# Kernel tuning notes

Hardware: AMD Instinct MI355X
Metric: run time of the kernel (lower is better)

Reference implementation:

```python
import jax, jax.numpy as jnp
import numpy as np

N = 100000   # nodes
E = 1600000  # edges
D_IN = 128
H = 64
L = 3        # num SAGE layers
G = 512      # graphs in batch


def setup_inputs() -> dict:
    key = jax.random.key(0)
    ks = jax.random.split(key, 12)
    s = 0.05
    return {
        "x": jax.random.normal(ks[0], (N, D_IN), dtype=jnp.float32),
        "edge_index": jax.random.randint(ks[1], (2, E), 0, N, dtype=jnp.int64),
        "edge_attr": jax.random.normal(ks[2], (E, 1), dtype=jnp.float32),
        "batch": jnp.sort(jax.random.randint(ks[3], (N,), 0, G, dtype=jnp.int64)),
        "W0": jax.random.normal(ks[4], (D_IN, H), dtype=jnp.float32) * s,
        "b0": jnp.zeros((H,), dtype=jnp.float32),
        "Wl": jax.random.normal(ks[5], (L, H, H), dtype=jnp.float32) * s,  # lin_l (aggregated neighbors), has bias
        "bl": jnp.zeros((L, H), dtype=jnp.float32),
        "Wr": jax.random.normal(ks[6], (L, H, H), dtype=jnp.float32) * s,  # lin_r (root), no bias
        "W1": jax.random.normal(ks[7], (H, H), dtype=jnp.float32) * s,
        "b1": jnp.zeros((H,), dtype=jnp.float32),
    }


def reference(x, edge_index, edge_attr, batch, W0, b0, Wl, bl, Wr, W1, b1):
    # edge_attr is accepted but unused, matching the torch module.
    h = jax.nn.relu(x @ W0 + b0)                    # [N, H]
    src, dst = edge_index[0], edge_index[1]
    ones_e = jnp.ones((E,), dtype=h.dtype)
    deg = jax.ops.segment_sum(ones_e, dst, num_segments=N)
    deg = jnp.clip(deg, 1.0)[:, None]               # avoid div by zero (PyG mean -> 0 for isolated)
    for i in range(L):
        # SAGEConv: mean-aggregate source features onto targets, then lin_l(agg)+lin_r(h)
        agg = jax.ops.segment_sum(h[src], dst, num_segments=N) / deg  # [N, H]
        h = jax.nn.relu(agg @ Wl[i] + bl[i] + h @ Wr[i])
    # global_mean_pool over batch ids
    cnt = jax.ops.segment_sum(jnp.ones((N,), dtype=h.dtype), batch, num_segments=G)
    pooled = jax.ops.segment_sum(h, batch, num_segments=G) / jnp.clip(cnt, 1.0)[:, None]  # [G, H]
    return pooled @ W1 + b1                          # [G, H]
```

## Files before the change

### kernel.cpp

```cpp
#include <hip/hip_runtime.h>
#include <hip/hip_bf16.h>

#define NN 100000
#define NE 1600000
#define DIN 128
#define NG 512
#define MAXD 64
#define NBUK 391
#define BCAP 5120
#define CHUNK ((NE + NBUK - 1) / NBUK)
#define NTILE ((NN + 63) >> 6)

typedef __attribute__((ext_vector_type(8))) __bf16 bf16x8;
typedef __attribute__((ext_vector_type(4))) float f32x4;

static __device__ __forceinline__ unsigned short bfhi(float f) {
    __hip_bfloat16 h = __float2bfloat16(f);
    return *reinterpret_cast<unsigned short*>(&h);
}
static __device__ __forceinline__ float bf2f(unsigned short u) {
    unsigned v = (unsigned)u << 16;
    return __uint_as_float(v);
}
static __device__ __forceinline__ bf16x8 ldfrag(const void* p) {
    bf16x8 r;
    __builtin_memcpy(&r, p, 16);
    return r;
}
static __device__ __forceinline__ int swz(int a) {
    return a ^ (((a >> 8) & 3) << 5) ^ (((a >> 12) & 3) << 4);
}


#define GB 256
__global__ void __launch_bounds__(512) k_front(const int* __restrict__ src,
                                               const int* __restrict__ dst,
                                               int* __restrict__ cursor,
                                               unsigned int* __restrict__ bucket,
                                               const float* __restrict__ x,
                                               const float* __restrict__ W0,
                                               const float* __restrict__ b0,
                                               float* __restrict__ h) {
    __shared__ unsigned short sS[2 * 8192];
    __shared__ int lcnt[NBUK];
    __shared__ int lbase[NBUK];
    if (blockIdx.x < NBUK) {
        for (int i = threadIdx.x; i < NBUK; i += 512) lcnt[i] = 0;
        __syncthreads();
        int e0 = blockIdx.x * CHUNK;
        int e1 = min(e0 + CHUNK, NE);
        for (int e = e0 + (int)threadIdx.x; e < e1; e += 512)
            atomicAdd(&lcnt[dst[e] >> 8], 1);
        __syncthreads();
        for (int i = threadIdx.x; i < NBUK; i += 512) {
            int c = lcnt[i];
            lbase[i] = c ? atomicAdd(&cursor[i], c) : 0;
            lcnt[i] = 0;
        }
        __syncthreads();
        for (int e = e0 + (int)threadIdx.x; e < e1; e += 512) {
            int d = dst[e];
            int s = src[e];
            int bk = d >> 8;
            int pos = lbase[bk] + atomicAdd(&lcnt[bk], 1);
            if (pos < BCAP)
                bucket[(size_t)bk * BCAP + pos] = ((unsigned)s << 8) | (unsigned)(d & 255);
        }
    } else {
        unsigned short* sP0 = sS;
        unsigned short* sP1 = sS + 8192;
        for (int i = threadIdx.x; i < 8192; i += 512) {
            int k = i >> 6, c = i & 63;
            int slot = ((k >> 5) << 2) | (c >> 4);
            int ln   = (((k >> 3) & 3) << 4) | (c & 15);
            int ba   = swz((((((slot << 6) | ln) << 3) | (k & 7)) << 1));
            float w0 = W0[i];
            unsigned short hh = bfhi(w0);
            *(unsigned short*)((char*)sP0 + ba) = hh;
            *(unsigned short*)((char*)sP1 + ba) = bfhi(w0 - bf2f(hh));
        }
        __syncthreads();
        int lane = threadIdx.x & 63;
        int wv   = threadIdx.x >> 6;
        int cb   = wv & 3;
        int rbh  = wv >> 2;
        int col  = (cb << 4) | (lane & 15);
        float bj = b0[col];
        int r0   = (lane >> 4) << 2;
        bf16x8 Bh[4], Bl[4];
#pragma unroll
        for (int ks = 0; ks < 4; ++ks) {
            int bb = swz(((((ks << 2) | cb) << 6) | lane) << 4);
            Bh[ks] = ldfrag((const char*)sP0 + bb);
            Bl[ks] = ldfrag((const char*)sP1 + bb);
        }
        for (int t = blockIdx.x - NBUK; t < NTILE; t += GB) {
            int n0 = t << 6;
            __syncthreads();
#pragma unroll
            for (int i = 0; i < 4; ++i) {
                int tau = (int)threadIdx.x + (i << 9);
                int r = tau >> 5, kq = tau & 31;
                int n = n0 + r;
                float4 v = make_float4(0.f, 0.f, 0.f, 0.f);
                if (n < NN) v = *(const float4*)(x + ((size_t)n << 7) + (kq << 2));
                int k0   = kq << 2;
                int slot = ((k0 >> 5) << 2) | (r >> 4);
                int ln   = (((k0 >> 3) & 3) << 4) | (r & 15);
                int ba   = swz((((((slot << 6) | ln) << 3) | (k0 & 7)) << 1));
                unsigned short h0 = bfhi(v.x), h1 = bfhi(v.y),
                               h2 = bfhi(v.z), h3 = bfhi(v.w);
                *(ushort4*)((char*)sP0 + ba) = make_ushort4(h0, h1, h2, h3);
                *(ushort4*)((char*)sP1 + ba) = make_ushort4(
                    bfhi(v.x - bf2f(h0)), bfhi(v.y - bf2f(h1)),
                    bfhi(v.z - bf2f(h2)), bfhi(v.w - bf2f(h3)));
            }
            __syncthreads();
            f32x4 acc[2] = {{0.f,0.f,0.f,0.f},{0.f,0.f,0.f,0.f}};
#pragma unroll
            for (int ks = 0; ks < 4; ++ks) {
#pragma unroll
                for (int rl = 0; rl < 2; ++rl) {
                    int rb = (rbh << 1) | rl;
                    int ab = swz(((((ks << 2) | rb) << 6) | lane) << 4);
                    bf16x8 ah = ldfrag((const char*)sP0 + ab);
                    bf16x8 al = ldfrag((const char*)sP1 + ab);
                    acc[rl] = __builtin_amdgcn_mfma_f32_16x16x32_bf16(ah, Bh[ks], acc[rl], 0, 0, 0);
                    acc[rl] = __builtin_amdgcn_mfma_f32_16x16x32_bf16(ah, Bl[ks], acc[rl], 0, 0, 0);
                    acc[rl] = __builtin_amdgcn_mfma_f32_16x16x32_bf16(al, Bh[ks], acc[rl], 0, 0, 0);
                }
            }
#pragma unroll
            for (int rl = 0; rl < 2; ++rl) {
                int rb = (rbh << 1) | rl;
#pragma unroll
                for (int reg = 0; reg < 4; ++reg) {
                    int row = (rb << 4) + r0 + reg;
                    int n = n0 + row;
                    if (n < NN)
                        h[((size_t)n << 6) + col] = fmaxf(acc[rl][reg] + bj, 0.f);
                }
            }
        }
    }
}

__device__ __forceinline__ void gemmLR_mfma(unsigned short* sS,
                                            int tid, int nblk, int bidx,
                                            float* __restrict__ h_r,
                                            __hip_bfloat16* __restrict__ g,
                                            const float* __restrict__ Wl,
                                            const float* __restrict__ bl,
                                            const float* __restrict__ Wr) {
    unsigned short* sP0 = sS;
    unsigned short* sP1 = sS + 4096;
    int lane = tid & 63;
    int cb   = tid >> 6;
    bf16x8 BLh[2], BLl[2], BRh[2], BRl[2];
    for (int i = tid; i < 4096; i += 256) {
        int k = i >> 6, c = i & 63;
        int slot = ((k >> 5) << 2) | (c >> 4);
        int ln   = (((k >> 3) & 3) << 4) | (c & 15);
        int ba   = swz((((((slot << 6) | ln) << 3) | (k & 7)) << 1));
        float w = Wl[i];
        unsigned short hh = bfhi(w);
        *(unsigned short*)((char*)sP0 + ba) = hh;
        *(unsigned short*)((char*)sP1 + ba) = bfhi(w - bf2f(hh));
    }
    __syncthreads();
#pragma unroll
    for (int ks = 0; ks < 2; ++ks) {
        int bb = swz(((((ks << 2) | cb) << 6) | lane) << 4);
        BLh[ks] = ldfrag((const char*)sP0 + bb);
        BLl[ks] = ldfrag((const char*)sP1 + bb);
    }
    __syncthreads();
    for (int i = tid; i < 4096; i += 256) {
        int k = i >> 6, c = i & 63;
        int slot = ((k >> 5) << 2) | (c >> 4);
        int ln   = (((k >> 3) & 3) << 4) | (c & 15);
        int ba   = swz((((((slot << 6) | ln) << 3) | (k & 7)) << 1));
        float w = Wr[i];
        unsigned short hh = bfhi(w);
        *(unsigned short*)((char*)sP0 + ba) = hh;
        *(unsigned short*)((char*)sP1 + ba) = bfhi(w - bf2f(hh));
    }
    __syncthreads();
#pragma unroll
    for (int ks = 0; ks < 2; ++ks) {
        int bb = swz(((((ks << 2) | cb) << 6) | lane) << 4);
        BRh[ks] = ldfrag((const char*)sP0 + bb);
        BRl[ks] = ldfrag((const char*)sP1 + bb);
    }
    int col = (cb << 4) | (lane & 15);
    float bj = bl[col];
    int r0  = (lane >> 4) << 2;
    unsigned short* gp = (unsigned short*)g;
    for (int t = bidx; t < NTILE; t += nblk) {
        int n0 = t << 6;
        __syncthreads();
#pragma unroll
        for (int i = 0; i < 4; ++i) {
            int tau = tid + (i << 8);
            int r = tau >> 4, kq = tau & 15;
            int n = n0 + r;
            float4 v = make_float4(0.f, 0.f, 0.f, 0.f);
            if (n < NN) v = *(const float4*)(h_r + ((size_t)n << 6) + (kq << 2));
            int k0   = kq << 2;
            int slot = ((k0 >> 5) << 2) | (r >> 4);
            int ln   = (((k0 >> 3) & 3) << 4) | (r & 15);
            int ba   = swz((((((slot << 6) | ln) << 3) | (k0 & 7)) << 1));
            unsigned short h0 = bfhi(v.x), h1 = bfhi(v.y),
                           h2 = bfhi(v.z), h3 = bfhi(v.w);
            *(ushort4*)((char*)sP0 + ba) = make_ushort4(h0, h1, h2, h3);
            *(ushort4*)((char*)sP1 + ba) = make_ushort4(
                bfhi(v.x - bf2f(h0)), bfhi(v.y - bf2f(h1)),
                bfhi(v.z - bf2f(h2)), bfhi(v.w - bf2f(h3)));
        }
        __syncthreads();
        f32x4 accl[4] = {{0.f,0.f,0.f,0.f},{0.f,0.f,0.f,0.f},
                         {0.f,0.f,0.f,0.f},{0.f,0.f,0.f,0.f}};
        f32x4 accr[4] = {{0.f,0.f,0.f,0.f},{0.f,0.f,0.f,0.f},
                         {0.f,0.f,0.f,0.f},{0.f,0.f,0.f,0.f}};
#pragma unroll
        for (int ks = 0; ks < 2; ++ks) {
#pragma unroll
            for (int rb = 0; rb < 4; ++rb) {
                int ab = swz(((((ks << 2) | rb) << 6) | lane) << 4);
                bf16x8 ah = ldfrag((const char*)sP0 + ab);
                bf16x8 al = ldfrag((const char*)sP1 + ab);
                accl[rb] = __builtin_amdgcn_mfma_f32_16x16x32_bf16(ah, BLh[ks], accl[rb], 0, 0, 0);
                accl[rb] = __builtin_amdgcn_mfma_f32_16x16x32_bf16(ah, BLl[ks], accl[rb], 0, 0, 0);
                accl[rb] = __builtin_amdgcn_mfma_f32_16x16x32_bf16(al, BLh[ks], accl[rb], 0, 0, 0);
                accr[rb] = __builtin_amdgcn_mfma_f32_16x16x32_bf16(ah, BRh[ks], accr[rb], 0, 0, 0);
                accr[rb] = __builtin_amdgcn_mfma_f32_16x16x32_bf16(ah, BRl[ks], accr[rb], 0, 0, 0);
                accr[rb] = __builtin_amdgcn_mfma_f32_16x16x32_bf16(al, BRh[ks], accr[rb], 0, 0, 0);
            }
        }
#pragma unroll
        for (int rb = 0; rb < 4; ++rb) {
#pragma unroll
            for (int reg = 0; reg < 4; ++reg) {
                int row = (rb << 4) + r0 + reg;
                int n = n0 + row;
                if (n < NN) {
                    size_t o = ((size_t)n << 6) + col;
                    gp[o]  = bfhi(accl[rb][reg]);
                    h_r[o] = accr[rb][reg] + bj;
                }
            }
        }
    }
}

#define MGB 512
__global__ void __launch_bounds__(256) k_mid(const unsigned int* __restrict__ bucket,
                                             const int* __restrict__ cursor,
                                             int* __restrict__ cnt,
                                             int* __restrict__ ell,
                                             float* __restrict__ h_r,
                                             __hip_bfloat16* __restrict__ g,
                                             const float* __restrict__ Wl,
                                             const float* __restrict__ bl,
                                             const float* __restrict__ Wr) {
    __shared__ unsigned short sS[2 * 4096];
    __shared__ int lc[256];
    if (blockIdx.x < NBUK) {
        lc[threadIdx.x] = 0;
        int b = blockIdx.x;
        __syncthreads();
        int m = min(cursor[b], BCAP);
        const unsigned int* bp = bucket + (size_t)b * BCAP;
        for (int i = threadIdx.x; i < m; i += 256) {
            unsigned v = bp[i];
            int dlo = (int)(v & 255u);
            int s   = (int)(v >> 8);
            int p   = atomicAdd(&lc[dlo], 1);
            if (p < MAXD)
                ell[(((size_t)b << 8) + dlo) * MAXD + p] = s;
        }
        __syncthreads();
        int n = (b << 8) + (int)threadIdx.x;
        if (n < NN) cnt[n] = lc[threadIdx.x];
    } else {
        gemmLR_mfma(sS, threadIdx.x, MGB, blockIdx.x - NBUK, h_r, g, Wl, bl, Wr);
    }
}

#define ACCU(U) { \
    a0 += __uint_as_float((U).x << 16); a1 += __uint_as_float((U).x & 0xffff0000u); \
    a2 += __uint_as_float((U).y << 16); a3 += __uint_as_float((U).y & 0xffff0000u); \
    a4 += __uint_as_float((U).z << 16); a5 += __uint_as_float((U).z & 0xffff0000u); \
    a6 += __uint_as_float((U).w << 16); a7 += __uint_as_float((U).w & 0xffff0000u); }

#define FB 512
__global__ void __launch_bounds__(512) k_gg(const uint4* __restrict__ gin,
                                            float* __restrict__ rA,
                                            unsigned short* __restrict__ gout,
                                            const int* __restrict__ cnt,
                                            const int* __restrict__ ell,
                                            const float* __restrict__ Wl,
                                            const float* __restrict__ bl,
                                            const float* __restrict__ Wr) {
    __shared__ unsigned short sS[2 * 4096];
    unsigned short* sP0 = sS;
    unsigned short* sP1 = sS + 4096;
    int tid = (int)threadIdx.x;
    int lane = tid & 63;
    int w    = tid >> 6;
    int cb   = w & 3;
    int rbh  = w >> 2;
    bf16x8 BLh[2], BLl[2], BRh[2], BRl[2];
    for (int i = tid; i < 4096; i += 512) {
        int k = i >> 6, c = i & 63;
        int slot = ((k >> 5) << 2) | (c >> 4);
        int ln   = (((k >> 3) & 3) << 4) | (c & 15);
        int ba   = swz((((((slot << 6) | ln) << 3) | (k & 7)) << 1));
        float wv_ = Wl[i];
        unsigned short hh = bfhi(wv_);
        *(unsigned short*)((char*)sP0 + ba) = hh;
        *(unsigned short*)((char*)sP1 + ba) = bfhi(wv_ - bf2f(hh));
    }
    __syncthreads();
#pragma unroll
    for (int ks = 0; ks < 2; ++ks) {
        int bb = swz(((((ks << 2) | cb) << 6) | lane) << 4);
        BLh[ks] = ldfrag((const char*)sP0 + bb);
        BLl[ks] = ldfrag((const char*)sP1 + bb);
    }
    __syncthreads();
    for (int i = tid; i < 4096; i += 512) {
        int k = i >> 6, c = i & 63;
        int slot = ((k >> 5) << 2) | (c >> 4);
        int ln   = (((k >> 3) & 3) << 4) | (c & 15);
        int ba   = swz((((((slot << 6) | ln) << 3) | (k & 7)) << 1));
        float wv_ = Wr[i];
        unsigned short hh = bfhi(wv_);
        *(unsigned short*)((char*)sP0 + ba) = hh;
        *(unsigned short*)((char*)sP1 + ba) = bfhi(wv_ - bf2f(hh));
    }
    __syncthreads();
#pragma unroll
    for (int ks = 0; ks < 2; ++ks) {
        int bb = swz(((((ks << 2) | cb) << 6) | lane) << 4);
        BRh[ks] = ldfrag((const char*)sP0 + bb);
        BRl[ks] = ldfrag((const char*)sP1 + bb);
    }
    int col = (cb << 4) | (lane & 15);
    float bj = bl[col];
    int r0  = (lane >> 4) << 2;
    int o   = lane >> 3;
    int c8  = lane & 7;
    for (int t = blockIdx.x; t < NTILE; t += FB) {
        int n0t = t << 6;
        int myn = n0t + (w << 3) + o;
        int d = (myn < NN) ? cnt[myn] : 0;
        int dc = min(d, MAXD);
        int dm = max(dc, __shfl_xor(dc, 8));
        dm     = max(dm, __shfl_xor(dm, 16));
        dm     = max(dm, __shfl_xor(dm, 32));
        int iters = (dm + 7) & ~7;
        const int* er = ell + ((size_t)min(myn, NN - 1) << 6) + (c8 << 3);
        int4 l0 = *(const int4*)er;
        int4 l1 = *(const int4*)(er + 4);
        float a0=0.f,a1=0.f,a2=0.f,a3=0.f,a4=0.f,a5=0.f,a6=0.f,a7=0.f;
        for (int j0 = 0; j0 < iters; j0 += 8) {
            int sl = (o << 3) | (j0 >> 3);
            int i0 = __shfl(l0.x, sl);
            int i1 = __shfl(l0.y, sl);
            int i2 = __shfl(l0.z, sl);
            int i3 = __shfl(l0.w, sl);
            int i4 = __shfl(l1.x, sl);
            int i5 = __shfl(l1.y, sl);
            int i6 = __shfl(l1.z, sl);
            int i7 = __shfl(l1.w, sl);
            i0 = (j0 + 0 < d) ? i0 : NN;
            i1 = (j0 + 1 < d) ? i1 : NN;
            i2 = (j0 + 2 < d) ? i2 : NN;
            i3 = (j0 + 3 < d) ? i3 : NN;
            i4 = (j0 + 4 < d) ? i4 : NN;
            i5 = (j0 + 5 < d) ? i5 : NN;
            i6 = (j0 + 6 < d) ? i6 : NN;
            i7 = (j0 + 7 < d) ? i7 : NN;
            uint4 u0 = gin[(size_t)i0 * 8 + c8];
            uint4 u1 = gin[(size_t)i1 * 8 + c8];
            uint4 u2 = gin[(size_t)i2 * 8 + c8];
            uint4 u3 = gin[(size_t)i3 * 8 + c8];
            uint4 u4 = gin[(size_t)i4 * 8 + c8];
            uint4 u5 = gin[(size_t)i5 * 8 + c8];
            uint4 u6 = gin[(size_t)i6 * 8 + c8];
            uint4 u7 = gin[(size_t)i7 * 8 + c8];
            ACCU(u0); ACCU(u1); ACCU(u2); ACCU(u3);
            ACCU(u4); ACCU(u5); ACCU(u6); ACCU(u7);
        }
        float4 rv0 = make_float4(0.f,0.f,0.f,0.f), rv1 = rv0;
        if (myn < NN) {
            float inv = 1.0f / fmaxf((float)d, 1.0f);
            const float4* rp = (const float4*)(rA + ((size_t)myn << 6) + (c8 << 3));
            rv0 = rp[0]; rv1 = rp[1];
            rv0.x = fmaxf(fmaf(a0, inv, rv0.x), 0.0f);
            rv0.y = fmaxf(fmaf(a1, inv, rv0.y), 0.0f);
            rv0.z = fmaxf(fmaf(a2, inv, rv0.z), 0.0f);
            rv0.w = fmaxf(fmaf(a3, inv, rv0.w), 0.0f);
            rv1.x = fmaxf(fmaf(a4, inv, rv1.x), 0.0f);
            rv1.y = fmaxf(fmaf(a5, inv, rv1.y), 0.0f);
            rv1.z = fmaxf(fmaf(a6, inv, rv1.z), 0.0f);
            rv1.w = fmaxf(fmaf(a7, inv, rv1.w), 0.0f);
        }
        __syncthreads();
        {
            int rr = (w << 3) + o;
#pragma unroll
            for (int half = 0; half < 2; ++half) {
                float4 v = half ? rv1 : rv0;
                int k0 = (c8 << 3) + (half << 2);
                int slot = ((k0 >> 5) << 2) | (rr >> 4);
                int ln   = (((k0 >> 3) & 3) << 4) | (rr & 15);
                int ba   = swz((((((slot << 6) | ln) << 3) | (k0 & 7)) << 1));
                unsigned short h0 = bfhi(v.x), h1 = bfhi(v.y),
                               h2 = bfhi(v.z), h3 = bfhi(v.w);
                *(ushort4*)((char*)sP0 + ba) = make_ushort4(h0, h1, h2, h3);
                *(ushort4*)((char*)sP1 + ba) = make_ushort4(
                    bfhi(v.x - bf2f(h0)), bfhi(v.y - bf2f(h1)),
                    bfhi(v.z - bf2f(h2)), bfhi(v.w - bf2f(h3)));
            }
        }
        __syncthreads();
        f32x4 accl[2] = {{0.f,0.f,0.f,0.f},{0.f,0.f,0.f,0.f}};
        f32x4 accr[2] = {{0.f,0.f,0.f,0.f},{0.f,0.f,0.f,0.f}};
#pragma unroll
        for (int ks = 0; ks < 2; ++ks) {
#pragma unroll
            for (int rl = 0; rl < 2; ++rl) {
                int rb = (rbh << 1) | rl;
                int ab = swz(((((ks << 2) | rb) << 6) | lane) << 4);
                bf16x8 ah = ldfrag((const char*)sP0 + ab);
                bf16x8 al = ldfrag((const char*)sP1 + ab);
                accl[rl] = __builtin_amdgcn_mfma_f32_16x16x32_bf16(ah, BLh[ks], accl[rl], 0, 0, 0);
                accl[rl] = __builtin_amdgcn_mfma_f32_16x16x32_bf16(ah, BLl[ks], accl[rl], 0, 0, 0);
                accl[rl] = __builtin_amdgcn_mfma_f32_16x16x32_bf16(al, BLh[ks], accl[rl], 0, 0, 0);
                accr[rl] = __builtin_amdgcn_mfma_f32_16x16x32_bf16(ah, BRh[ks], accr[rl], 0, 0, 0);
                accr[rl] = __builtin_amdgcn_mfma_f32_16x16x32_bf16(ah, BRl[ks], accr[rl], 0, 0, 0);
                accr[rl] = __builtin_amdgcn_mfma_f32_16x16x32_bf16(al, BRh[ks], accr[rl], 0, 0, 0);
            }
        }
#pragma unroll
        for (int rl = 0; rl < 2; ++rl) {
            int rb = (rbh << 1) | rl;
#pragma unroll
            for (int reg = 0; reg < 4; ++reg) {
                int row = (rb << 4) + r0 + reg;
                int n = n0t + row;
                if (n < NN) {
                    size_t off = ((size_t)n << 6) + col;
                    gout[off] = bfhi(accl[rl][reg]);
                    rA[off]   = accr[rl][reg] + bj;
                }
            }
        }
    }
}

__global__ void __launch_bounds__(256) k_gpool(const uint4* __restrict__ g4,
                                               const float* __restrict__ rA,
                                               const int* __restrict__ cnt,
                                               const int* __restrict__ ell,
                                               const int* __restrict__ batch,
                                               float* __restrict__ pool,
                                               float* __restrict__ cntg) {
    int lane = threadIdx.x & 63;
    int o    = lane >> 3;
    int c8   = lane & 7;
    int wv = __builtin_amdgcn_readfirstlane((int)((blockIdx.x * 256 + threadIdx.x) >> 6));
    int nw = (gridDim.x * 256) >> 6;
    for (int p = wv; p < NN / 8; p += nw) {
        int myn = 8 * p + o;
        int d   = cnt[myn];
        int dc  = min(d, MAXD);
        int dm  = max(dc, __shfl_xor(dc, 8));
        dm      = max(dm, __shfl_xor(dm, 16));
        dm      = max(dm, __shfl_xor(dm, 32));
        int iters = (dm + 7) & ~7;
        const int* er = ell + ((size_t)myn << 6) + (c8 << 3);
        int4 l0 = *(const int4*)er;
        int4 l1 = *(const int4*)(er + 4);
        float a0=0.f,a1=0.f,a2=0.f,a3=0.f,a4=0.f,a5=0.f,a6=0.f,a7=0.f;
        for (int j0 = 0; j0 < iters; j0 += 8) {
            int sl = (o << 3) | (j0 >> 3);
            int i0 = __shfl(l0.x, sl);
            int i1 = __shfl(l0.y, sl);
            int i2 = __shfl(l0.z, sl);
            int i3 = __shfl(l0.w, sl);
            int i4 = __shfl(l1.x, sl);
            int i5 = __shfl(l1.y, sl);
            int i6 = __shfl(l1.z, sl);
            int i7 = __shfl(l1.w, sl);
            i0 = (j0 + 0 < d) ? i0 : NN;
            i1 = (j0 + 1 < d) ? i1 : NN;
            i2 = (j0 + 2 < d) ? i2 : NN;
            i3 = (j0 + 3 < d) ? i3 : NN;
            i4 = (j0 + 4 < d) ? i4 : NN;
            i5 = (j0 + 5 < d) ? i5 : NN;
            i6 = (j0 + 6 < d) ? i6 : NN;
            i7 = (j0 + 7 < d) ? i7 : NN;
            uint4 u0 = g4[(size_t)i0 * 8 + c8];
            uint4 u1 = g4[(size_t)i1 * 8 + c8];
            uint4 u2 = g4[(size_t)i2 * 8 + c8];
            uint4 u3 = g4[(size_t)i3 * 8 + c8];
            uint4 u4 = g4[(size_t)i4 * 8 + c8];
            uint4 u5 = g4[(size_t)i5 * 8 + c8];
            uint4 u6 = g4[(size_t)i6 * 8 + c8];
            uint4 u7 = g4[(size_t)i7 * 8 + c8];
            ACCU(u0); ACCU(u1); ACCU(u2); ACCU(u3);
            ACCU(u4); ACCU(u5); ACCU(u6); ACCU(u7);
        }
        float inv = 1.0f / fmaxf((float)d, 1.0f);
        const float4* rp = (const float4*)(rA + ((size_t)myn << 6) + (c8 << 3));
        float4 rv0 = rp[0], rv1 = rp[1];
        float v0 = fmaxf(fmaf(a0, inv, rv0.x), 0.0f);
        float v1 = fmaxf(fmaf(a1, inv, rv0.y), 0.0f);
        float v2 = fmaxf(fmaf(a2, inv, rv0.z), 0.0f);
        float v3 = fmaxf(fmaf(a3, inv, rv0.w), 0.0f);
        float v4 = fmaxf(fmaf(a4, inv, rv1.x), 0.0f);
        float v5 = fmaxf(fmaf(a5, inv, rv1.y), 0.0f);
        float v6 = fmaxf(fmaf(a6, inv, rv1.z), 0.0f);
        float v7 = fmaxf(fmaf(a7, inv, rv1.w), 0.0f);
        int b  = batch[myn];
        int b0 = __shfl(b, c8);
        if (__all(b == b0)) {
#pragma unroll
            for (int m = 8; m <= 32; m <<= 1) {
                v0 += __shfl_xor(v0, m); v1 += __shfl_xor(v1, m);
                v2 += __shfl_xor(v2, m); v3 += __shfl_xor(v3, m);
                v4 += __shfl_xor(v4, m); v5 += __shfl_xor(v5, m);
                v6 += __shfl_xor(v6, m); v7 += __shfl_xor(v7, m);
            }
            if (o == 0) {
                float* pb = pool + ((size_t)b0 << 6) + (c8 << 3);
                atomicAdd(pb + 0, v0); atomicAdd(pb + 1, v1);
                atomicAdd(pb + 2, v2); atomicAdd(pb + 3, v3);
                atomicAdd(pb + 4, v4); atomicAdd(pb + 5, v5);
                atomicAdd(pb + 6, v6); atomicAdd(pb + 7, v7);
                if (c8 == 0) atomicAdd(&cntg[b0], 8.0f);
            }
        } else {
            float* pb = pool + ((size_t)b << 6) + (c8 << 3);
            atomicAdd(pb + 0, v0); atomicAdd(pb + 1, v1);
            atomicAdd(pb + 2, v2); atomicAdd(pb + 3, v3);
            atomicAdd(pb + 4, v4); atomicAdd(pb + 5, v5);
            atomicAdd(pb + 6, v6); atomicAdd(pb + 7, v7);
            if (c8 == 0) atomicAdd(&cntg[b], 1.0f);
        }
    }
}

__global__ void __launch_bounds__(256) k_out(const float* __restrict__ pool,
                                             const float* __restrict__ cntg,
                                             const float* __restrict__ W1,
                                             const float* __restrict__ b1,
                                             float* __restrict__ out) {
    __shared__ float sW[64 * 64];
    for (int i = threadIdx.x; i < 64 * 64; i += 256) sW[i] = W1[i];
    __syncthreads();
    int lane = threadIdx.x & 63;
    int wid  = (blockIdx.x * 256 + threadIdx.x) >> 6;
    int nw   = (gridDim.x * 256) >> 6;
    for (int gidx = wid; gidx < NG; gidx += nw) {
        float ic = 1.0f / fmaxf(cntg[gidx], 1.0f);
        float acc = 0.0f;
#pragma unroll
        for (int k = 0; k < 64; ++k)
            acc = fmaf(pool[(size_t)gidx * 64 + k], sW[k * 64 + lane], acc);
        out[(size_t)gidx * 64 + lane] = fmaf(acc, ic, b1[lane]);
    }
}

extern "C" void kernel_launch(void* const* d_in, const int* in_sizes, int n_in,
                              void* d_out, int out_size, void* d_ws, size_t ws_size,
                              hipStream_t stream) {
    const float* x     = (const float*)d_in[0];
    const int*   ei    = (const int*)d_in[1];
    const int*   batch = (const int*)d_in[3];
    const float* W0    = (const float*)d_in[4];
    const float* b0    = (const float*)d_in[5];
    const float* Wl    = (const float*)d_in[6];
    const float* bl    = (const float*)d_in[7];
    const float* Wr    = (const float*)d_in[8];
    const float* W1    = (const float*)d_in[9];
    const float* b1    = (const float*)d_in[10];
    float* out = (float*)d_out;

    char* ws = (char*)d_ws;
    size_t off = 0;
    auto alloc = [&](size_t bytes) -> void* {
        void* p = ws + off;
        off += (bytes + 255) & ~(size_t)255;
        return p;
    };
    float*          A  = (float*)alloc((size_t)NN * 64 * 4);
    unsigned short* G0 = (unsigned short*)alloc((size_t)NN * 128);
    size_t z1start = off;
    (void)alloc(256);
    unsigned short* G1 = (unsigned short*)alloc((size_t)NN * 128);
    size_t z2start = off;
    (void)alloc(256);
    int*   cursor = (int*)alloc((size_t)NBUK * 4);
    float* pool   = (float*)alloc((size_t)NG * 64 * 4);
    float* cntg   = (float*)alloc((size_t)NG * 4);
    size_t z2len = off - z2start;
    int*          ell    = (int*)alloc((size_t)NN * MAXD * 4);
    unsigned int* bucket = (unsigned int*)alloc((size_t)NBUK * BCAP * 4);
    int*          cnt    = (int*)alloc((size_t)NN * 4);

    const int* src = ei;
    const int* dst = ei + NE;

    hipMemsetAsync(ws + z1start, 0, 256, stream);
    hipMemsetAsync(ws + z2start, 0, z2len, stream);

    k_front<<<NBUK + GB, 512, 0, stream>>>(src, dst, cursor, bucket, x, W0, b0, A);
    k_mid<<<NBUK + MGB, 256, 0, stream>>>(bucket, cursor, cnt, ell, A,
                                          (__hip_bfloat16*)G0, Wl, bl, Wr);
    k_gg<<<FB, 512, 0, stream>>>((const uint4*)G0, A, G1, cnt, ell,
                                 Wl + (size_t)1 * 64 * 64, bl + 64, Wr + (size_t)1 * 64 * 64);
    k_gg<<<FB, 512, 0, stream>>>((const uint4*)G1, A, G0, cnt, ell,
                                 Wl + (size_t)2 * 64 * 64, bl + 128, Wr + (size_t)2 * 64 * 64);
    k_gpool<<<3125, 256, 0, stream>>>((const uint4*)G0, A, cnt, ell, batch, pool, cntg);

    k_out<<<128, 256, 0, stream>>>(pool, cntg, W1, b1, out);
}
```

Measured before the change: 387.4 us.

## Fuse layer-0 Wl/Wr projection into input GEMM tiles of k_front

```diff
diff --git a/kernel.cpp b/kernel.cpp
--- a/kernel.cpp
+++ b/kernel.cpp
@@ -40,8 +40,13 @@
                                                const float* __restrict__ x,
                                                const float* __restrict__ W0,
                                                const float* __restrict__ b0,
-                                               float* __restrict__ h) {
-    __shared__ unsigned short sS[2 * 8192];
+                                               const float* __restrict__ Wl0,
+                                               const float* __restrict__ bl0,
+                                               const float* __restrict__ Wr0,
+                                               unsigned short* __restrict__ gout,
+                                               float* __restrict__ rA) {
+    __shared__ unsigned short sW0[2 * 8192];
+    __shared__ unsigned short sS2[2 * 8192];
     __shared__ int lcnt[NBUK];
     __shared__ int lbase[NBUK];
     if (blockIdx.x < NBUK) {
@@ -67,39 +72,73 @@
                 bucket[(size_t)bk * BCAP + pos] = ((unsigned)s << 8) | (unsigned)(d & 255);
         }
     } else {
-        unsigned short* sP0 = sS;
-        unsigned short* sP1 = sS + 8192;
-        for (int i = threadIdx.x; i < 8192; i += 512) {
+        int tid = (int)threadIdx.x;
+        unsigned short* w0h = sW0;
+        unsigned short* w0l = sW0 + 8192;
+        unsigned short* sP0 = sS2;
+        unsigned short* sP1 = sS2 + 8192;
+        unsigned short* hP0 = sS2;
+        unsigned short* hP1 = sS2 + 4096;
+        for (int i = tid; i < 8192; i += 512) {
             int k = i >> 6, c = i & 63;
             int slot = ((k >> 5) << 2) | (c >> 4);
             int ln   = (((k >> 3) & 3) << 4) | (c & 15);
             int ba   = swz((((((slot << 6) | ln) << 3) | (k & 7)) << 1));
-            float w0 = W0[i];
-            unsigned short hh = bfhi(w0);
-            *(unsigned short*)((char*)sP0 + ba) = hh;
-            *(unsigned short*)((char*)sP1 + ba) = bfhi(w0 - bf2f(hh));
-        }
-        __syncthreads();
-        int lane = threadIdx.x & 63;
-        int wv   = threadIdx.x >> 6;
+            float w = W0[i];
+            unsigned short hh = bfhi(w);
+            *(unsigned short*)((char*)w0h + ba) = hh;
+            *(unsigned short*)((char*)w0l + ba) = bfhi(w - bf2f(hh));
+        }
+        int lane = tid & 63;
+        int wv   = tid >> 6;
         int cb   = wv & 3;
         int rbh  = wv >> 2;
         int col  = (cb << 4) | (lane & 15);
-        float bj = b0[col];
+        float bj  = b0[col];
+        float bj2 = bl0[col];
         int r0   = (lane >> 4) << 2;
-        bf16x8 Bh[4], Bl[4];
-#pragma unroll
-        for (int ks = 0; ks < 4; ++ks) {
+        bf16x8 BLh[2], BLl[2], BRh[2], BRl[2];
+        for (int i = tid; i < 4096; i += 512) {
+            int k = i >> 6, c = i & 63;
+            int slot = ((k >> 5) << 2) | (c >> 4);
+            int ln   = (((k >> 3) & 3) << 4) | (c & 15);
+            int ba   = swz((((((slot << 6) | ln) << 3) | (k & 7)) << 1));
+            float w = Wl0[i];
+            unsigned short hh = bfhi(w);
+            *(unsigned short*)((char*)hP0 + ba) = hh;
+            *(unsigned short*)((char*)hP1 + ba) = bfhi(w - bf2f(hh));
+        }
+        __syncthreads();
+#pragma unroll
+        for (int ks = 0; ks < 2; ++ks) {
             int bb = swz(((((ks << 2) | cb) << 6) | lane) << 4);
-            Bh[ks] = ldfrag((const char*)sP0 + bb);
-            Bl[ks] = ldfrag((const char*)sP1 + bb);
+            BLh[ks] = ldfrag((const char*)hP0 + bb);
+            BLl[ks] = ldfrag((const char*)hP1 + bb);
+        }
+        __syncthreads();
+        for (int i = tid; i < 4096; i += 512) {
+            int k = i >> 6, c = i & 63;
+            int slot = ((k >> 5) << 2) | (c >> 4);
+            int ln   = (((k >> 3) & 3) << 4) | (c & 15);
+            int ba   = swz((((((slot << 6) | ln) << 3) | (k & 7)) << 1));
+            float w = Wr0[i];
+            unsigned short hh = bfhi(w);
+            *(unsigned short*)((char*)hP0 + ba) = hh;
+            *(unsigned short*)((char*)hP1 + ba) = bfhi(w - bf2f(hh));
+        }
+        __syncthreads();
+#pragma unroll
+        for (int ks = 0; ks < 2; ++ks) {
+            int bb = swz(((((ks << 2) | cb) << 6) | lane) << 4);
+            BRh[ks] = ldfrag((const char*)hP0 + bb);
+            BRl[ks] = ldfrag((const char*)hP1 + bb);
         }
         for (int t = blockIdx.x - NBUK; t < NTILE; t += GB) {
             int n0 = t << 6;
             __syncthreads();
 #pragma unroll
             for (int i = 0; i < 4; ++i) {
-                int tau = (int)threadIdx.x + (i << 9);
+                int tau = tid + (i << 9);
                 int r = tau >> 5, kq = tau & 31;
                 int n = n0 + r;
                 float4 v = make_float4(0.f, 0.f, 0.f, 0.f);
@@ -119,15 +158,53 @@
             f32x4 acc[2] = {{0.f,0.f,0.f,0.f},{0.f,0.f,0.f,0.f}};
 #pragma unroll
             for (int ks = 0; ks < 4; ++ks) {
+                int bb = swz(((((ks << 2) | cb) << 6) | lane) << 4);
+                bf16x8 bh  = ldfrag((const char*)w0h + bb);
+                bf16x8 bl_ = ldfrag((const char*)w0l + bb);
 #pragma unroll
                 for (int rl = 0; rl < 2; ++rl) {
                     int rb = (rbh << 1) | rl;
                     int ab = swz(((((ks << 2) | rb) << 6) | lane) << 4);
                     bf16x8 ah = ldfrag((const char*)sP0 + ab);
                     bf16x8 al = ldfrag((const char*)sP1 + ab);
-                    acc[rl] = __builtin_amdgcn_mfma_f32_16x16x32_bf16(ah, Bh[ks], acc[rl], 0, 0, 0);
-                    acc[rl] = __builtin_amdgcn_mfma_f32_16x16x32_bf16(ah, Bl[ks], acc[rl], 0, 0, 0);
-                    acc[rl] = __builtin_amdgcn_mfma_f32_16x16x32_bf16(al, Bh[ks], acc[rl], 0, 0, 0);
+                    acc[rl] = __builtin_amdgcn_mfma_f32_16x16x32_bf16(ah, bh,  acc[rl], 0, 0, 0);
+                    acc[rl] = __builtin_amdgcn_mfma_f32_16x16x32_bf16(ah, bl_, acc[rl], 0, 0, 0);
+                    acc[rl] = __builtin_amdgcn_mfma_f32_16x16x32_bf16(al, bh,  acc[rl], 0, 0, 0);
+                }
+            }
+            __syncthreads();
+#pragma unroll
+            for (int rl = 0; rl < 2; ++rl) {
+                int rb = (rbh << 1) | rl;
+#pragma unroll
+                for (int reg = 0; reg < 4; ++reg) {
+                    int row = (rb << 4) + r0 + reg;
+                    float v = fmaxf(acc[rl][reg] + bj, 0.f);
+                    int slot = ((col >> 5) << 2) | rb;
+                    int ln   = (((col >> 3) & 3) << 4) | (row & 15);
+                    int ba   = swz((((((slot << 6) | ln) << 3) | (col & 7)) << 1));
+                    unsigned short hh = bfhi(v);
+                    *(unsigned short*)((char*)hP0 + ba) = hh;
+                    *(unsigned short*)((char*)hP1 + ba) = bfhi(v - bf2f(hh));
+                }
+            }
+            __syncthreads();
+            f32x4 accl[2] = {{0.f,0.f,0.f,0.f},{0.f,0.f,0.f,0.f}};
+            f32x4 accr[2] = {{0.f,0.f,0.f,0.f},{0.f,0.f,0.f,0.f}};
+#pragma unroll
+            for (int ks = 0; ks < 2; ++ks) {
+#pragma unroll
+                for (int rl = 0; rl < 2; ++rl) {
+                    int rb = (rbh << 1) | rl;
+                    int ab = swz(((((ks << 2) | rb) << 6) | lane) << 4);
+                    bf16x8 ah = ldfrag((const char*)hP0 + ab);
+                    bf16x8 al = ldfrag((const char*)hP1 + ab);
+                    accl[rl] = __builtin_amdgcn_mfma_f32_16x16x32_bf16(ah, BLh[ks], accl[rl], 0, 0, 0);
+                    accl[rl] = __builtin_amdgcn_mfma_f32_16x16x32_bf16(ah, BLl[ks], accl[rl], 0, 0, 0);
+                    accl[rl] = __builtin_amdgcn_mfma_f32_16x16x32_bf16(al, BLh[ks], accl[rl], 0, 0, 0);
+                    accr[rl] = __builtin_amdgcn_mfma_f32_16x16x32_bf16(ah, BRh[ks], accr[rl], 0, 0, 0);
+                    accr[rl] = __builtin_amdgcn_mfma_f32_16x16x32_bf16(ah, BRl[ks], accr[rl], 0, 0, 0);
+                    accr[rl] = __builtin_amdgcn_mfma_f32_16x16x32_bf16(al, BRh[ks], accr[rl], 0, 0, 0);
                 }
             }
 #pragma unroll
@@ -137,154 +214,38 @@
                 for (int reg = 0; reg < 4; ++reg) {
                     int row = (rb << 4) + r0 + reg;
                     int n = n0 + row;
-                    if (n < NN)
-                        h[((size_t)n << 6) + col] = fmaxf(acc[rl][reg] + bj, 0.f);
+                    if (n < NN) {
+                        size_t off = ((size_t)n << 6) + col;
+                        gout[off] = bfhi(accl[rl][reg]);
+                        rA[off]   = accr[rl][reg] + bj2;
+                    }
                 }
             }
         }
     }
 }
 
-__device__ __forceinline__ void gemmLR_mfma(unsigned short* sS,
-                                            int tid, int nblk, int bidx,
-                                            float* __restrict__ h_r,
-                                            __hip_bfloat16* __restrict__ g,
-                                            const float* __restrict__ Wl,
-                                            const float* __restrict__ bl,
-                                            const float* __restrict__ Wr) {
-    unsigned short* sP0 = sS;
-    unsigned short* sP1 = sS + 4096;
-    int lane = tid & 63;
-    int cb   = tid >> 6;
-    bf16x8 BLh[2], BLl[2], BRh[2], BRl[2];
-    for (int i = tid; i < 4096; i += 256) {
-        int k = i >> 6, c = i & 63;
-        int slot = ((k >> 5) << 2) | (c >> 4);
-        int ln   = (((k >> 3) & 3) << 4) | (c & 15);
-        int ba   = swz((((((slot << 6) | ln) << 3) | (k & 7)) << 1));
-        float w = Wl[i];
-        unsigned short hh = bfhi(w);
-        *(unsigned short*)((char*)sP0 + ba) = hh;
-        *(unsigned short*)((char*)sP1 + ba) = bfhi(w - bf2f(hh));
-    }
+__global__ void __launch_bounds__(256) k_mide(const unsigned int* __restrict__ bucket,
+                                              const int* __restrict__ cursor,
+                                              int* __restrict__ cnt,
+                                              int* __restrict__ ell) {
+    __shared__ int lc[256];
+    lc[threadIdx.x] = 0;
+    int b = blockIdx.x;
     __syncthreads();
-#pragma unroll
-    for (int ks = 0; ks < 2; ++ks) {
-        int bb = swz(((((ks << 2) | cb) << 6) | lane) << 4);
-        BLh[ks] = ldfrag((const char*)sP0 + bb);
-        BLl[ks] = ldfrag((const char*)sP1 + bb);
+    int m = min(cursor[b], BCAP);
+    const unsigned int* bp = bucket + (size_t)b * BCAP;
+    for (int i = threadIdx.x; i < m; i += 256) {
+        unsigned v = bp[i];
+        int dlo = (int)(v & 255u);
+        int s   = (int)(v >> 8);
+        int p   = atomicAdd(&lc[dlo], 1);
+        if (p < MAXD)
+            ell[(((size_t)b << 8) + dlo) * MAXD + p] = s;
     }
     __syncthreads();
-    for (int i = tid; i < 4096; i += 256) {
-        int k = i >> 6, c = i & 63;
-        int slot = ((k >> 5) << 2) | (c >> 4);
-        int ln   = (((k >> 3) & 3) << 4) | (c & 15);
-        int ba   = swz((((((slot << 6) | ln) << 3) | (k & 7)) << 1));
-        float w = Wr[i];
-        unsigned short hh = bfhi(w);
-        *(unsigned short*)((char*)sP0 + ba) = hh;
-        *(unsigned short*)((char*)sP1 + ba) = bfhi(w - bf2f(hh));
-    }
-    __syncthreads();
-#pragma unroll
-    for (int ks = 0; ks < 2; ++ks) {
-        int bb = swz(((((ks << 2) | cb) << 6) | lane) << 4);
-        BRh[ks] = ldfrag((const char*)sP0 + bb);
-        BRl[ks] = ldfrag((const char*)sP1 + bb);
-    }
-    int col = (cb << 4) | (lane & 15);
-    float bj = bl[col];
-    int r0  = (lane >> 4) << 2;
-    unsigned short* gp = (unsigned short*)g;
-    for (int t = bidx; t < NTILE; t += nblk) {
-        int n0 = t << 6;
-        __syncthreads();
-#pragma unroll
-        for (int i = 0; i < 4; ++i) {
-            int tau = tid + (i << 8);
-            int r = tau >> 4, kq = tau & 15;
-            int n = n0 + r;
-            float4 v = make_float4(0.f, 0.f, 0.f, 0.f);
-            if (n < NN) v = *(const float4*)(h_r + ((size_t)n << 6) + (kq << 2));
-            int k0   = kq << 2;
-            int slot = ((k0 >> 5) << 2) | (r >> 4);
-            int ln   = (((k0 >> 3) & 3) << 4) | (r & 15);
-            int ba   = swz((((((slot << 6) | ln) << 3) | (k0 & 7)) << 1));
-            unsigned short h0 = bfhi(v.x), h1 = bfhi(v.y),
-                           h2 = bfhi(v.z), h3 = bfhi(v.w);
-            *(ushort4*)((char*)sP0 + ba) = make_ushort4(h0, h1, h2, h3);
-            *(ushort4*)((char*)sP1 + ba) = make_ushort4(
-                bfhi(v.x - bf2f(h0)), bfhi(v.y - bf2f(h1)),
-                bfhi(v.z - bf2f(h2)), bfhi(v.w - bf2f(h3)));
-        }
-        __syncthreads();
-        f32x4 accl[4] = {{0.f,0.f,0.f,0.f},{0.f,0.f,0.f,0.f},
-                         {0.f,0.f,0.f,0.f},{0.f,0.f,0.f,0.f}};
-        f32x4 accr[4] = {{0.f,0.f,0.f,0.f},{0.f,0.f,0.f,0.f},
-                         {0.f,0.f,0.f,0.f},{0.f,0.f,0.f,0.f}};
-#pragma unroll
-        for (int ks = 0; ks < 2; ++ks) {
-#pragma unroll
-            for (int rb = 0; rb < 4; ++rb) {
-                int ab = swz(((((ks << 2) | rb) << 6) | lane) << 4);
-                bf16x8 ah = ldfrag((const char*)sP0 + ab);
-                bf16x8 al = ldfrag((const char*)sP1 + ab);
-                accl[rb] = __builtin_amdgcn_mfma_f32_16x16x32_bf16(ah, BLh[ks], accl[rb], 0, 0, 0);
-                accl[rb] = __builtin_amdgcn_mfma_f32_16x16x32_bf16(ah, BLl[ks], accl[rb], 0, 0, 0);
-                accl[rb] = __builtin_amdgcn_mfma_f32_16x16x32_bf16(al, BLh[ks], accl[rb], 0, 0, 0);
-                accr[rb] = __builtin_amdgcn_mfma_f32_16x16x32_bf16(ah, BRh[ks], accr[rb], 0, 0, 0);
-                accr[rb] = __builtin_amdgcn_mfma_f32_16x16x32_bf16(ah, BRl[ks], accr[rb], 0, 0, 0);
-                accr[rb] = __builtin_amdgcn_mfma_f32_16x16x32_bf16(al, BRh[ks], accr[rb], 0, 0, 0);
-            }
-        }
-#pragma unroll
-        for (int rb = 0; rb < 4; ++rb) {
-#pragma unroll
-            for (int reg = 0; reg < 4; ++reg) {
-                int row = (rb << 4) + r0 + reg;
-                int n = n0 + row;
-                if (n < NN) {
-                    size_t o = ((size_t)n << 6) + col;
-                    gp[o]  = bfhi(accl[rb][reg]);
-                    h_r[o] = accr[rb][reg] + bj;
-                }
-            }
-        }
-    }
-}
-
-#define MGB 512
-__global__ void __launch_bounds__(256) k_mid(const unsigned int* __restrict__ bucket,
-                                             const int* __restrict__ cursor,
-                                             int* __restrict__ cnt,
-                                             int* __restrict__ ell,
-                                             float* __restrict__ h_r,
-                                             __hip_bfloat16* __restrict__ g,
-                                             const float* __restrict__ Wl,
-                                             const float* __restrict__ bl,
-                                             const float* __restrict__ Wr) {
-    __shared__ unsigned short sS[2 * 4096];
-    __shared__ int lc[256];
-    if (blockIdx.x < NBUK) {
-        lc[threadIdx.x] = 0;
-        int b = blockIdx.x;
-        __syncthreads();
-        int m = min(cursor[b], BCAP);
-        const unsigned int* bp = bucket + (size_t)b * BCAP;
-        for (int i = threadIdx.x; i < m; i += 256) {
-            unsigned v = bp[i];
-            int dlo = (int)(v & 255u);
-            int s   = (int)(v >> 8);
-            int p   = atomicAdd(&lc[dlo], 1);
-            if (p < MAXD)
-                ell[(((size_t)b << 8) + dlo) * MAXD + p] = s;
-        }
-        __syncthreads();
-        int n = (b << 8) + (int)threadIdx.x;
-        if (n < NN) cnt[n] = lc[threadIdx.x];
-    } else {
-        gemmLR_mfma(sS, threadIdx.x, MGB, blockIdx.x - NBUK, h_r, g, Wl, bl, Wr);
-    }
+    int n = (b << 8) + (int)threadIdx.x;
+    if (n < NN) cnt[n] = lc[threadIdx.x];
 }
 
 #define ACCU(U) { \
@@ -618,9 +579,9 @@
     hipMemsetAsync(ws + z1start, 0, 256, stream);
     hipMemsetAsync(ws + z2start, 0, z2len, stream);
 
-    k_front<<<NBUK + GB, 512, 0, stream>>>(src, dst, cursor, bucket, x, W0, b0, A);
-    k_mid<<<NBUK + MGB, 256, 0, stream>>>(bucket, cursor, cnt, ell, A,
-                                          (__hip_bfloat16*)G0, Wl, bl, Wr);
+    k_front<<<NBUK + GB, 512, 0, stream>>>(src, dst, cursor, bucket, x, W0, b0,
+                                           Wl, bl, Wr, G0, A);
+    k_mide<<<NBUK, 256, 0, stream>>>(bucket, cursor, cnt, ell);
     k_gg<<<FB, 512, 0, stream>>>((const uint4*)G0, A, G1, cnt, ell,
                                  Wl + (size_t)1 * 64 * 64, bl + 64, Wr + (size_t)1 * 64 * 64);
     k_gg<<<FB, 512, 0, stream>>>((const uint4*)G1, A, G0, cnt, ell,
```

After: 372.4 us (median of 2 runs). 3.9% less time.
